# Kernel tuning notes

Measured on AMD Instinct MI355X. Metric: run time of the kernel, lower is better.

Reference implementation:

```python
import jax, jax.numpy as jnp
import numpy as np

V, E, H, L = 32000, 300, 512, 2
B, S, T1 = 32, 256, 65  # T1 = target len + 1


def setup_inputs() -> dict:
    key = jax.random.key(0)
    ks = jax.random.split(key, 24)
    sd = 0.05
    n = lambda k, shp: (jax.random.normal(k, shp, dtype=jnp.float32) * sd)
    embed = n(ks[0], (V, E)).at[0].set(0.0)  # padding_idx=0 row zeroed
    inp = {
        "encoder_output": jax.random.normal(ks[1], (B, S, 2 * H), dtype=jnp.float32),
        "encoder_hidden": jax.random.normal(ks[2], (2 * L, B, H), dtype=jnp.float32),
        "output_words": jax.random.randint(ks[3], (B, T1), 0, V),
        "embed": embed,
        # GRU layer 0 (input E) and layer 1 (input H); torch gate order r,z,n
        "Wih0": n(ks[4], (3 * H, E)), "Whh0": n(ks[5], (3 * H, H)),
        "bih0": n(ks[6], (3 * H,)), "bhh0": n(ks[7], (3 * H,)),
        "Wih1": n(ks[8], (3 * H, H)), "Whh1": n(ks[9], (3 * H, H)),
        "bih1": n(ks[10], (3 * H,)), "bhh1": n(ks[11], (3 * H,)),
        # Luong general attention: project encoder_output (2H) -> H
        "attn_W": n(ks[12], (H, 2 * H)), "attn_b": n(ks[13], (H,)),
        # attention_wight: Linear(3H, 3H)
        "aw_W": n(ks[14], (3 * H, 3 * H)), "aw_b": n(ks[15], (3 * H,)),
        # out: Linear(3H, V)
        "out_W": n(ks[16], (V, 3 * H)), "out_b": n(ks[17], (V,)),
    }
    return inp


def _gru_layer(x, h0, Wih, Whh, bih, bhh):
    # x: (B,T,in), h0: (B,H) -> (B,T,H)
    Hd = h0.shape[-1]
    gi = jnp.einsum("bti,gi->btg", x, Wih) + bih  # precompute input gates

    def step(h, gi_t):
        gh = h @ Whh.T + bhh
        r = jax.nn.sigmoid(gi_t[:, :Hd] + gh[:, :Hd])
        z = jax.nn.sigmoid(gi_t[:, Hd:2 * Hd] + gh[:, Hd:2 * Hd])
        nn_ = jnp.tanh(gi_t[:, 2 * Hd:] + r * gh[:, 2 * Hd:])
        h = (1.0 - z) * nn_ + z * h
        return h, h

    _, ys = jax.lax.scan(step, h0, jnp.swapaxes(gi, 0, 1))
    return jnp.swapaxes(ys, 0, 1)


def reference(encoder_output, encoder_hidden, output_words, embed,
              Wih0, Whh0, bih0, bhh0, Wih1, Whh1, bih1, bhh1,
              attn_W, attn_b, aw_W, aw_b, out_W, out_b):
    Bsz = output_words.shape[0]
    src = output_words[:, :-1]  # teacher forcing with ratio 1 => always source
    x = jax.nn.relu(embed[src])  # (B,T,E)
    eh = encoder_hidden.reshape(2, L, Bsz, H)
    h0 = eh[0] + eh[1]  # (L,B,H) sum of bidirectional halves
    h = _gru_layer(x, h0[0], Wih0, Whh0, bih0, bhh0)
    h = _gru_layer(h, h0[1], Wih1, Whh1, bih1, bhh1)  # (B,T,H)
    # Luong general attention over encoder_output (B,S,2H)
    proj = jnp.einsum("bsd,hd->bsh", encoder_output, attn_W) + attn_b
    scores = jnp.einsum("bth,bsh->bts", h, proj)
    attn = jax.nn.softmax(scores, axis=-1)
    ctx = jnp.einsum("bts,bsd->btd", attn, encoder_output)  # (B,T,2H)
    cat = jnp.concatenate([h, ctx], axis=-1)  # (B,T,3H)
    o = jax.nn.relu(jnp.einsum("btc,oc->bto", cat, aw_W) + aw_b)  # dropout = eval identity
    logits = jnp.einsum("btc,vc->btv", o, out_W) + out_b  # (B,T,V)
    return logits
```

## Files before the change

### kernel.cpp

```cpp
#include <hip/hip_runtime.h>

typedef _Float16 half8 __attribute__((ext_vector_type(8)));
typedef float f32x4 __attribute__((ext_vector_type(4)));
typedef _Float16 half2_t __attribute__((ext_vector_type(2)));
typedef const void __attribute__((address_space(1)))* gas_cptr;
typedef void __attribute__((address_space(3)))* las_ptr;

__device__ __forceinline__ unsigned short f2h(float f) {
  return __builtin_bit_cast(unsigned short, (_Float16)f);
}
__device__ __forceinline__ unsigned int packh2(float a, float b) {
  unsigned short lo = __builtin_bit_cast(unsigned short, (_Float16)a);
  unsigned short hi = __builtin_bit_cast(unsigned short, (_Float16)b);
  return (unsigned int)lo | ((unsigned int)hi << 16);
}
__device__ __forceinline__ float fdot2f(unsigned int a, unsigned int b, float c) {
#if __has_builtin(__builtin_amdgcn_fdot2)
  return __builtin_amdgcn_fdot2(__builtin_bit_cast(half2_t, a),
                                __builtin_bit_cast(half2_t, b), c, false);
#else
  half2_t ha = __builtin_bit_cast(half2_t, a), hb = __builtin_bit_cast(half2_t, b);
  return c + (float)ha[0] * (float)hb[0] + (float)ha[1] * (float)hb[1];
#endif
}
__device__ __forceinline__ float fsigm(float x) {
  x = fminf(15.f, fmaxf(-15.f, x));
  return 1.f / (1.f + __expf(-x));
}
__device__ __forceinline__ float ftanhf(float x) {
  x = fminf(15.f, fmaxf(-15.f, x));
  float e = __expf(-2.f * x);
  return (1.f - e) / (1.f + e);
}
__device__ __forceinline__ void stage16(const void* g, void* l) {
  __builtin_amdgcn_global_load_lds((gas_cptr)g, (las_ptr)l, 16, 0, 0);
}

__global__ __launch_bounds__(256) void cvt4(const float4* __restrict__ in,
                                            ushort4* __restrict__ out, int n4) {
  for (int i = blockIdx.x * 256 + threadIdx.x; i < n4; i += gridDim.x * 256) {
    float4 v = in[i];
    ushort4 r;
    r.x = f2h(v.x); r.y = f2h(v.y); r.z = f2h(v.z); r.w = f2h(v.w);
    out[i] = r;
  }
}

__global__ __launch_bounds__(256) void cvt_pad_wih0(const float* __restrict__ W,
                                                    unsigned short* __restrict__ o) {
  int idx = blockIdx.x * 256 + threadIdx.x;
  if (idx >= 1536 * 320) return;
  int r = idx / 320, c = idx - r * 320;
  float v = (c < 300) ? W[(long)r * 300 + c] : 0.f;
  o[idx] = f2h(v);
}

__global__ __launch_bounds__(256) void embed_relu(const int* __restrict__ words,
                                                  const float* __restrict__ emb,
                                                  unsigned short* __restrict__ x) {
  int idx = blockIdx.x * 256 + threadIdx.x;
  if (idx >= 2048 * 320) return;
  int row = idx / 320, e = idx - row * 320;
  int b = row >> 6, t = row & 63;
  int w = words[b * 65 + t];
  float v = 0.f;
  if (e < 300) v = fmaxf(emb[(long)w * 300 + e], 0.f);
  x[idx] = f2h(v);
}

__global__ __launch_bounds__(256) void h0_sum(const float* __restrict__ hid,
                                              float* __restrict__ h0) {
  int idx = blockIdx.x * 256 + threadIdx.x;
  if (idx >= 2 * 32 * 512) return;
  int l = idx >> 14, rem = idx & 16383;
  h0[idx] = hid[l * 16384 + rem] + hid[(2 + l) * 16384 + rem];
}

__global__ __launch_bounds__(256) void pack_whh8(const float* __restrict__ W,
                                                 unsigned int* __restrict__ o) {
  int f = blockIdx.x * 256 + threadIdx.x;
  if (f >= 393216) return;
  int i = f & 63;
  int s = (f >> 6) & 3;
  int row = f >> 8;
  const float* p = W + (long)row * 512 + s * 128 + 2 * i;
  o[f] = packh2(p[0], p[1]);
}

__global__ __launch_bounds__(256) void slots_init(const float* __restrict__ h0,
                                                  unsigned long long* __restrict__ s0,
                                                  unsigned long long* __restrict__ s1) {
  const long N = 65L * 32 * 256;
  for (long i = (long)blockIdx.x * 256 + threadIdx.x; i < 2 * N;
       i += (long)gridDim.x * 256) {
    int l = (int)(i / N);
    long r = i - (long)l * N;
    unsigned long long* dst = l ? s1 : s0;
    if (r < 32 * 256) {
      int b = (int)(r >> 8), p = (int)(r & 255);
      unsigned int pv = packh2(h0[l * 16384 + b * 512 + 2 * p],
                               h0[l * 16384 + b * 512 + 2 * p + 1]);
      dst[r] = (unsigned long long)pv | ((unsigned long long)(~pv) << 32);
    } else {
      dst[r] = 0ULL;
    }
  }
}

__global__ void transpose_enc(const float* __restrict__ e, unsigned short* __restrict__ et) {
  __shared__ float t[32][33];
  int d0 = blockIdx.x * 32, s0 = blockIdx.y * 32, b = blockIdx.z;
  const float* eb = e + (long)b * 256 * 1024;
  for (int i = threadIdx.y; i < 32; i += 8)
    t[i][threadIdx.x] = eb[(long)(s0 + i) * 1024 + d0 + threadIdx.x];
  __syncthreads();
  unsigned short* eo = et + (long)b * 1024 * 256;
  for (int i = threadIdx.y; i < 32; i += 8)
    eo[(long)(d0 + i) * 256 + s0 + threadIdx.x] = f2h(t[threadIdx.x][i]);
}

__global__ __launch_bounds__(256) void softmax_rows(const float* __restrict__ s,
                                                    unsigned short* __restrict__ a) {
  int row = blockIdx.x * 4 + (threadIdx.x >> 6);
  int lane = threadIdx.x & 63;
  const float* sr = s + (long)row * 256;
  float v[4], m = -1e30f;
#pragma unroll
  for (int i = 0; i < 4; i++) { v[i] = sr[lane + 64 * i]; m = fmaxf(m, v[i]); }
#pragma unroll
  for (int o = 32; o; o >>= 1) m = fmaxf(m, __shfl_xor(m, o));
  float sum = 0.f;
#pragma unroll
  for (int i = 0; i < 4; i++) { v[i] = __expf(v[i] - m); sum += v[i]; }
#pragma unroll
  for (int o = 32; o; o >>= 1) sum += __shfl_xor(sum, o);
  float inv = 1.f / sum;
#pragma unroll
  for (int i = 0; i < 4; i++) a[(long)row * 256 + lane + 64 * i] = f2h(v[i] * inv);
}

template <int BM, int BN, int WM, int WN, bool OUT_F16, bool HAS_BIAS, bool RELU>
__global__ __launch_bounds__(WM * WN * 64) void gemm_bt(
    const unsigned short* __restrict__ A, const unsigned short* __restrict__ B,
    void* __restrict__ Cv, const float* __restrict__ bias, int K, int lda, int ldb,
    int ldc, long sA, long sB, long sC) {
  constexpr int NT = WM * WN * 64;
  constexpr int IA = (BM * 32) / (NT * 8);
  constexpr int IB = (BN * 32) / (NT * 8);
  static_assert((BM * 32) % (NT * 8) == 0 && (BN * 32) % (NT * 8) == 0, "staging");
  __shared__ __align__(16) unsigned short As[BM * 32];
  __shared__ __align__(16) unsigned short Bs[BN * 32];
  const int tid = threadIdx.x;
  const int wave = tid >> 6, lane = tid & 63;
  const int wm = wave / WN, wn = wave % WN;
  const int lr = lane & 15, lq = lane >> 4;
  const long z = blockIdx.z;
  const unsigned short* Ab = A + z * sA + (long)blockIdx.y * BM * lda;
  const unsigned short* Bb = B + z * sB + (long)blockIdx.x * BN * ldb;

  f32x4 acc[4][4];
#pragma unroll
  for (int i = 0; i < 4; i++)
#pragma unroll
    for (int j = 0; j < 4; j++) acc[i][j] = (f32x4){0.f, 0.f, 0.f, 0.f};

  for (int k0 = 0; k0 < K; k0 += 32) {
#pragma unroll
    for (int i = 0; i < IA; i++) {
      int flat = (i * NT + tid) * 8;
      int r = flat >> 5, c = flat & 31;
      stage16(Ab + (long)r * lda + k0 + c, &As[(i * NT + wave * 64) * 8]);
    }
#pragma unroll
    for (int i = 0; i < IB; i++) {
      int flat = (i * NT + tid) * 8;
      int r = flat >> 5, c = flat & 31;
      stage16(Bb + (long)r * ldb + k0 + c, &Bs[(i * NT + wave * 64) * 8]);
    }
    __syncthreads();
    half8 af[4], bf[4];
#pragma unroll
    for (int t = 0; t < 4; t++)
      af[t] = *(const half8*)&As[(wm * 64 + t * 16 + lr) * 32 + lq * 8];
#pragma unroll
    for (int t = 0; t < 4; t++)
      bf[t] = *(const half8*)&Bs[(wn * 64 + t * 16 + lr) * 32 + lq * 8];
#pragma unroll
    for (int ti = 0; ti < 4; ti++)
#pragma unroll
      for (int tj = 0; tj < 4; tj++)
        acc[ti][tj] = __builtin_amdgcn_mfma_f32_16x16x32_f16(af[ti], bf[tj],
                                                             acc[ti][tj], 0, 0, 0);
    __syncthreads();
  }

  const long crow0 = (long)blockIdx.y * BM + wm * 64;
  const long ccol0 = (long)blockIdx.x * BN + wn * 64;
  float bv[4];
  if constexpr (HAS_BIAS) {
#pragma unroll
    for (int tj = 0; tj < 4; tj++) bv[tj] = bias[ccol0 + tj * 16 + lr];
  }
#pragma unroll
  for (int ti = 0; ti < 4; ti++)
#pragma unroll
    for (int tj = 0; tj < 4; tj++) {
      long col = ccol0 + tj * 16 + lr;
#pragma unroll
      for (int r = 0; r < 4; r++) {
        long row = crow0 + ti * 16 + lq * 4 + r;
        float v = acc[ti][tj][r];
        if constexpr (HAS_BIAS) v += bv[tj];
        if constexpr (RELU) v = fmaxf(v, 0.f);
        if constexpr (OUT_F16)
          ((unsigned short*)Cv)[z * sC + row * ldc + col] = f2h(v);
        else
          ((float*)Cv)[z * sC + row * ldc + col] = v;
      }
    }
}

__global__ __launch_bounds__(256, 1) void gru_scan8(
    const float* __restrict__ gi,
    const unsigned int* __restrict__ wp,
    const float* __restrict__ bhh,
    const float* __restrict__ h0,
    unsigned long long* __restrict__ slots,
    unsigned short* __restrict__ out, int ldo) {
  const int b = blockIdx.x & 31;
  const int c = blockIdx.x >> 5;
  const int tid = threadIdx.x;
  const int ld = tid >> 2, s = tid & 3;
  const int dim = c * 64 + ld;
  __shared__ __align__(16) unsigned int hp[2][4 * 68];

  unsigned int w0[64], w1[64], w2[64];
  {
    const uint4* p0 = (const uint4*)(wp + ((long)(0 * 512 + dim) * 4 + s) * 64);
    const uint4* p1 = (const uint4*)(wp + ((long)(512 + dim) * 4 + s) * 64);
    const uint4* p2 = (const uint4*)(wp + ((long)(1024 + dim) * 4 + s) * 64);
#pragma unroll
    for (int i = 0; i < 16; i++) {
      uint4 v = p0[i];
      w0[4 * i] = v.x; w0[4 * i + 1] = v.y; w0[4 * i + 2] = v.z; w0[4 * i + 3] = v.w;
    }
#pragma unroll
    for (int i = 0; i < 16; i++) {
      uint4 v = p1[i];
      w1[4 * i] = v.x; w1[4 * i + 1] = v.y; w1[4 * i + 2] = v.z; w1[4 * i + 3] = v.w;
    }
#pragma unroll
    for (int i = 0; i < 16; i++) {
      uint4 v = p2[i];
      w2[4 * i] = v.x; w2[4 * i + 1] = v.y; w2[4 * i + 2] = v.z; w2[4 * i + 3] = v.w;
    }
  }
  const bool lead = (s == 0);
  float hprev = 0.f, br = 0.f, bz = 0.f, bn = 0.f;
  if (lead) {
    hprev = h0[b * 512 + dim];
    br = bhh[dim]; bz = bhh[512 + dim]; bn = bhh[1024 + dim];
  }

  for (int t = 0; t < 64; t++) {
    const long row = (long)b * 64 + t;
    float gr = 0.f, gz = 0.f, gn = 0.f;
    if (lead) {
      gr = gi[row * 1536 + dim];
      gz = gi[row * 1536 + 512 + dim];
      gn = gi[row * 1536 + 1024 + dim];
    }
    {
      const unsigned long long* sp = slots + ((long)t * 32 + b) * 256 + tid;
      unsigned long long v =
          __hip_atomic_load(sp, __ATOMIC_RELAXED, __HIP_MEMORY_SCOPE_AGENT);
      unsigned int guard = 0;
      while ((unsigned int)(v >> 32) != ~(unsigned int)v) {
        __builtin_amdgcn_s_sleep(1);
        v = __hip_atomic_load(sp, __ATOMIC_RELAXED, __HIP_MEMORY_SCOPE_AGENT);
        if (++guard > (1u << 20)) break;
      }
      hp[t & 1][(tid >> 6) * 68 + (tid & 63)] = (unsigned int)v;
    }
    __syncthreads();
    float ar = 0.f, az = 0.f, an = 0.f;
    const uint4* hv4 = (const uint4*)(hp[t & 1] + s * 68);
#pragma unroll
    for (int m = 0; m < 16; m++) {
      uint4 hv = hv4[m];
      ar = fdot2f(hv.x, w0[4 * m], ar);
      az = fdot2f(hv.x, w1[4 * m], az);
      an = fdot2f(hv.x, w2[4 * m], an);
      ar = fdot2f(hv.y, w0[4 * m + 1], ar);
      az = fdot2f(hv.y, w1[4 * m + 1], az);
      an = fdot2f(hv.y, w2[4 * m + 1], an);
      ar = fdot2f(hv.z, w0[4 * m + 2], ar);
      az = fdot2f(hv.z, w1[4 * m + 2], az);
      an = fdot2f(hv.z, w2[4 * m + 2], an);
      ar = fdot2f(hv.w, w0[4 * m + 3], ar);
      az = fdot2f(hv.w, w1[4 * m + 3], az);
      an = fdot2f(hv.w, w2[4 * m + 3], an);
    }
    ar += __shfl_xor(ar, 1); ar += __shfl_xor(ar, 2);
    az += __shfl_xor(az, 1); az += __shfl_xor(az, 2);
    an += __shfl_xor(an, 1); an += __shfl_xor(an, 2);
    float hn = 0.f;
    if (lead) {
      float r = fsigm(gr + br + ar);
      float zz = fsigm(gz + bz + az);
      float nn = ftanhf(gn + r * (an + bn));
      hn = (1.f - zz) * nn + zz * hprev;
      hprev = hn;
      out[row * ldo + dim] = f2h(hn);
    }
    float ho = __shfl_xor(hn, 4);
    if (lead && ((ld & 1) == 0)) {
      unsigned int pv = packh2(hn, ho);
      unsigned long long pw =
          (unsigned long long)pv | ((unsigned long long)(~pv) << 32);
      __hip_atomic_store(slots + ((long)(t + 1) * 32 + b) * 256 + c * 32 + (ld >> 1),
                         pw, __ATOMIC_RELAXED, __HIP_MEMORY_SCOPE_AGENT);
    }
  }
}

extern "C" void kernel_launch(void* const* d_in, const int* in_sizes, int n_in,
                              void* d_out, int out_size, void* d_ws, size_t ws_size,
                              hipStream_t stream) {
  const float* enc = (const float*)d_in[0];
  const float* ehid = (const float*)d_in[1];
  const int* words = (const int*)d_in[2];
  const float* embed = (const float*)d_in[3];
  const float* Wih0 = (const float*)d_in[4];
  const float* Whh0 = (const float*)d_in[5];
  const float* bih0 = (const float*)d_in[6];
  const float* bhh0 = (const float*)d_in[7];
  const float* Wih1 = (const float*)d_in[8];
  const float* Whh1 = (const float*)d_in[9];
  const float* bih1 = (const float*)d_in[10];
  const float* bhh1 = (const float*)d_in[11];
  const float* attW = (const float*)d_in[12];
  const float* attb = (const float*)d_in[13];
  const float* awW = (const float*)d_in[14];
  const float* awb = (const float*)d_in[15];
  const float* outW = (const float*)d_in[16];
  const float* outb = (const float*)d_in[17];
  float* out = (float*)d_out;

  char* ws = (char*)d_ws;
  size_t off = 0;
  auto alloc = [&](size_t bytes) {
    char* p = ws + off;
    off = (off + bytes + 255) & ~(size_t)255;
    return p;
  };
  unsigned short* xpad = (unsigned short*)alloc(2048ULL * 320 * 2);
  unsigned short* wih0p = (unsigned short*)alloc(1536ULL * 320 * 2);
  unsigned short* wih1b = (unsigned short*)alloc(1536ULL * 512 * 2);
  unsigned short* attwb = (unsigned short*)alloc(512ULL * 1024 * 2);
  unsigned short* awwb = (unsigned short*)alloc(1536ULL * 1536 * 2);
  unsigned short* outwb = (unsigned short*)alloc(32000ULL * 1536 * 2);
  unsigned short* encb = (unsigned short*)alloc(8192ULL * 1024 * 2);
  unsigned short* enct = (unsigned short*)alloc(32ULL * 1024 * 256 * 2);
  unsigned int* wp0 = (unsigned int*)alloc(393216ULL * 4);
  unsigned int* wp1 = (unsigned int*)alloc(393216ULL * 4);
  float* h0b = (float*)alloc(2ULL * 32 * 512 * 4);
  unsigned long long* slots0 = (unsigned long long*)alloc(65ULL * 32 * 256 * 8);
  unsigned long long* slots1 = (unsigned long long*)alloc(65ULL * 32 * 256 * 8);
  float* gi0 = (float*)alloc(2048ULL * 1536 * 4);
  float* gi1 = (float*)alloc(2048ULL * 1536 * 4);
  unsigned short* ys0 = (unsigned short*)alloc(2048ULL * 512 * 2);
  unsigned short* projb = (unsigned short*)alloc(8192ULL * 512 * 2);
  float* scores = (float*)alloc(2048ULL * 256 * 4);
  unsigned short* attnb = (unsigned short*)alloc(2048ULL * 256 * 2);
  unsigned short* catb = (unsigned short*)alloc(2048ULL * 1536 * 2);
  unsigned short* obuf = (unsigned short*)alloc(2048ULL * 1536 * 2);
  (void)ws_size; (void)in_sizes; (void)n_in; (void)out_size;

  cvt4<<<4096, 256, 0, stream>>>((const float4*)enc, (ushort4*)encb, 2097152);
  cvt4<<<1024, 256, 0, stream>>>((const float4*)attW, (ushort4*)attwb, 131072);
  cvt4<<<2048, 256, 0, stream>>>((const float4*)awW, (ushort4*)awwb, 589824);
  cvt4<<<4096, 256, 0, stream>>>((const float4*)outW, (ushort4*)outwb, 12288000);
  cvt4<<<768, 256, 0, stream>>>((const float4*)Wih1, (ushort4*)wih1b, 196608);
  cvt_pad_wih0<<<1920, 256, 0, stream>>>(Wih0, wih0p);
  transpose_enc<<<dim3(32, 8, 32), dim3(32, 8), 0, stream>>>(enc, enct);
  pack_whh8<<<1536, 256, 0, stream>>>(Whh0, wp0);
  pack_whh8<<<1536, 256, 0, stream>>>(Whh1, wp1);
  embed_relu<<<2560, 256, 0, stream>>>(words, embed, xpad);
  h0_sum<<<128, 256, 0, stream>>>(ehid, h0b);
  slots_init<<<4160, 256, 0, stream>>>(h0b, slots0, slots1);

  gemm_bt<128, 128, 2, 2, false, true, false><<<dim3(12, 16, 1), 256, 0, stream>>>(
      xpad, wih0p, gi0, bih0, 320, 320, 320, 1536, 0, 0, 0);
  gru_scan8<<<256, 256, 0, stream>>>(gi0, wp0, bhh0, h0b, slots0, ys0, 512);
  gemm_bt<128, 128, 2, 2, false, true, false><<<dim3(12, 16, 1), 256, 0, stream>>>(
      ys0, wih1b, gi1, bih1, 512, 512, 512, 1536, 0, 0, 0);
  gru_scan8<<<256, 256, 0, stream>>>(gi1, wp1, bhh1, h0b + 16384, slots1,
                                     catb, 1536);
  gemm_bt<128, 128, 2, 2, true, true, false><<<dim3(4, 64, 1), 256, 0, stream>>>(
      encb, attwb, projb, attb, 1024, 1024, 1024, 512, 0, 0, 0);
  gemm_bt<64, 128, 1, 2, false, false, false><<<dim3(2, 1, 32), 128, 0, stream>>>(
      catb, projb, scores, nullptr, 512, 1536, 512, 256,
      64L * 1536, 256L * 512, 64L * 256);
  softmax_rows<<<512, 256, 0, stream>>>(scores, attnb);
  gemm_bt<64, 128, 1, 2, true, false, false><<<dim3(8, 1, 32), 128, 0, stream>>>(
      attnb, enct, catb + 512, nullptr, 256, 256, 256, 1536,
      64L * 256, 1024L * 256, 64L * 1536);
  gemm_bt<128, 128, 2, 2, true, true, true><<<dim3(12, 16, 1), 256, 0, stream>>>(
      catb, awwb, obuf, awb, 1536, 1536, 1536, 1536, 0, 0, 0);
  gemm_bt<128, 128, 2, 2, false, true, false><<<dim3(250, 16, 1), 256, 0, stream>>>(
      obuf, outwb, out, outb, 1536, 1536, 1536, 32000, 0, 0, 0);
}
```

Before: 1.134 ms.

## Swizzle GEMM LDS layout and make M the fast grid dimension for vocab GEMM

Applies an XOR swizzle on the 8-element column chunk, keyed by row, both when staging A/B tiles into shared memory and when reading MFMA fragments. This is meant to cut LDS bank conflicts on the fragment loads. Separately, the large output-projection GEMM now runs with M-tiles on the fast grid axis, so consecutive blocks share the same out_W column tile. That should improve L2 reuse of the 32000x1536 weight matrix. The swizzle changes the global address each thread loads, which could slightly hurt coalescing within a row segment.

Result: no change. 1.115 ms (-1.6%).

```diff
diff --git a/kernel.cpp b/kernel.cpp
--- a/kernel.cpp
+++ b/kernel.cpp
@@ -139,7 +139,8 @@
   for (int i = 0; i < 4; i++) a[(long)row * 256 + lane + 64 * i] = f2h(v[i] * inv);
 }
 
-template <int BM, int BN, int WM, int WN, bool OUT_F16, bool HAS_BIAS, bool RELU>
+template <int BM, int BN, int WM, int WN, bool OUT_F16, bool HAS_BIAS, bool RELU,
+          bool MFAST = false>
 __global__ __launch_bounds__(WM * WN * 64) void gemm_bt(
     const unsigned short* __restrict__ A, const unsigned short* __restrict__ B,
     void* __restrict__ Cv, const float* __restrict__ bias, int K, int lda, int ldb,
@@ -155,8 +156,10 @@
   const int wm = wave / WN, wn = wave % WN;
   const int lr = lane & 15, lq = lane >> 4;
   const long z = blockIdx.z;
-  const unsigned short* Ab = A + z * sA + (long)blockIdx.y * BM * lda;
-  const unsigned short* Bb = B + z * sB + (long)blockIdx.x * BN * ldb;
+  const int bxN = MFAST ? blockIdx.y : blockIdx.x;
+  const int byM = MFAST ? blockIdx.x : blockIdx.y;
+  const unsigned short* Ab = A + z * sA + (long)byM * BM * lda;
+  const unsigned short* Bb = B + z * sB + (long)bxN * BN * ldb;
 
   f32x4 acc[4][4];
 #pragma unroll
@@ -169,22 +172,28 @@
     for (int i = 0; i < IA; i++) {
       int flat = (i * NT + tid) * 8;
       int r = flat >> 5, c = flat & 31;
-      stage16(Ab + (long)r * lda + k0 + c, &As[(i * NT + wave * 64) * 8]);
+      int cs = c ^ (((r >> 1) & 3) << 3);
+      stage16(Ab + (long)r * lda + k0 + cs, &As[(i * NT + wave * 64) * 8]);
     }
 #pragma unroll
     for (int i = 0; i < IB; i++) {
       int flat = (i * NT + tid) * 8;
       int r = flat >> 5, c = flat & 31;
-      stage16(Bb + (long)r * ldb + k0 + c, &Bs[(i * NT + wave * 64) * 8]);
+      int cs = c ^ (((r >> 1) & 3) << 3);
+      stage16(Bb + (long)r * ldb + k0 + cs, &Bs[(i * NT + wave * 64) * 8]);
     }
     __syncthreads();
     half8 af[4], bf[4];
 #pragma unroll
-    for (int t = 0; t < 4; t++)
-      af[t] = *(const half8*)&As[(wm * 64 + t * 16 + lr) * 32 + lq * 8];
-#pragma unroll
-    for (int t = 0; t < 4; t++)
-      bf[t] = *(const half8*)&Bs[(wn * 64 + t * 16 + lr) * 32 + lq * 8];
+    for (int t = 0; t < 4; t++) {
+      int ra = wm * 64 + t * 16 + lr;
+      af[t] = *(const half8*)&As[ra * 32 + ((lq ^ ((ra >> 1) & 3)) << 3)];
+    }
+#pragma unroll
+    for (int t = 0; t < 4; t++) {
+      int rb = wn * 64 + t * 16 + lr;
+      bf[t] = *(const half8*)&Bs[rb * 32 + ((lq ^ ((rb >> 1) & 3)) << 3)];
+    }
 #pragma unroll
     for (int ti = 0; ti < 4; ti++)
 #pragma unroll
@@ -194,8 +203,8 @@
     __syncthreads();
   }
 
-  const long crow0 = (long)blockIdx.y * BM + wm * 64;
-  const long ccol0 = (long)blockIdx.x * BN + wn * 64;
+  const long crow0 = (long)byM * BM + wm * 64;
+  const long ccol0 = (long)bxN * BN + wn * 64;
   float bv[4];
   if constexpr (HAS_BIAS) {
 #pragma unroll
@@ -408,6 +417,6 @@
       64L * 256, 1024L * 256, 64L * 1536);
   gemm_bt<128, 128, 2, 2, true, true, true><<<dim3(12, 16, 1), 256, 0, stream>>>(
       catb, awwb, obuf, awb, 1536, 1536, 1536, 1536, 0, 0, 0);
-  gemm_bt<128, 128, 2, 2, false, true, false><<<dim3(250, 16, 1), 256, 0, stream>>>(
+  gemm_bt<128, 128, 2, 2, false, true, false, true><<<dim3(16, 250, 1), 256, 0, stream>>>(
       obuf, outwb, out, outb, 1536, 1536, 1536, 32000, 0, 0, 0);
 }
```
